# Performance work log

Hardware: AMD Instinct MI355X
Metric: run time of the kernel (lower is better)

Reference implementation:

```python
import jax, jax.numpy as jnp
import numpy as np

N_NODES = 10000


def _sage_conv(x, src, dst, W_l, W_r, b):
    # mean aggregation of source features at destination nodes (PyG SAGEConv default)
    msg = x[src]                                             # [E, C_in]
    agg = jax.ops.segment_sum(msg, dst, num_segments=N_NODES)  # [N, C_in]
    cnt = jax.ops.segment_sum(jnp.ones((src.shape[0],), x.dtype), dst,
                              num_segments=N_NODES)
    mean = agg / jnp.maximum(cnt, 1.0)[:, None]              # isolated nodes -> 0
    return mean @ W_l + x @ W_r + b


def setup_inputs() -> dict:
    key = jax.random.key(0)
    ks = jax.random.split(key, 8)
    E = 640000
    x = jax.random.normal(ks[0], (N_NODES, 128), dtype=jnp.float32)
    edge_index = jax.random.randint(ks[1], (2, E), 0, N_NODES, dtype=jnp.int64)
    W1_l = jax.random.normal(ks[2], (128, 256), dtype=jnp.float32) * 0.05
    W1_r = jax.random.normal(ks[3], (128, 256), dtype=jnp.float32) * 0.05
    b1 = jnp.zeros((256,), dtype=jnp.float32)
    W2_l = jax.random.normal(ks[4], (256, 128), dtype=jnp.float32) * 0.05
    W2_r = jax.random.normal(ks[5], (256, 128), dtype=jnp.float32) * 0.05
    b2 = jnp.zeros((128,), dtype=jnp.float32)
    return {"x": x, "edge_index": edge_index, "W1_l": W1_l, "W1_r": W1_r,
            "b1": b1, "W2_l": W2_l, "W2_r": W2_r, "b2": b2}


def reference(x, edge_index, W1_l, W1_r, b1, W2_l, W2_r, b2):
    src, dst = edge_index[0], edge_index[1]
    h = jax.nn.relu(_sage_conv(x, src, dst, W1_l, W1_r, b1))
    out = _sage_conv(h, src, dst, W2_l, W2_r, b2)
    return out
```

## Files before the change

kernel.cpp:

```cpp
#include <hip/hip_runtime.h>

#define N_NODES 10000
#define HB 128

typedef unsigned int uint;
typedef unsigned short ushort;
typedef __attribute__((ext_vector_type(8))) short bf16x8;
typedef __attribute__((ext_vector_type(4))) float f32x4;

__device__ __forceinline__ ushort f2bf(float f) {
    uint b = __float_as_uint(f);
    b += 0x7fffu + ((b >> 16) & 1u);
    return (ushort)(b >> 16);
}

#define CAST_B 1250
#define TCAST_B 512

__global__ __launch_bounds__(256) void prep_kernel(const float* __restrict__ x,
                                                   const float* __restrict__ W1l,
                                                   const float* __restrict__ W1r,
                                                   const float* __restrict__ W2l,
                                                   const float* __restrict__ W2r,
                                                   const int* __restrict__ dst, int E, int chunk,
                                                   int* __restrict__ chunk_hist,
                                                   ushort* __restrict__ lrank,
                                                   ushort* __restrict__ xb,
                                                   ushort* __restrict__ W1T,
                                                   ushort* __restrict__ W2T,
                                                   int* __restrict__ aggv) {
    __shared__ int hist[N_NODES];
    int b = blockIdx.x;
    int t = threadIdx.x;
    if (b < HB) {
        int4* h4 = (int4*)hist;
        for (int i = t; i < N_NODES / 4; i += 256) h4[i] = make_int4(0, 0, 0, 0);
        __syncthreads();
        int e0 = b * chunk;
        int e1 = e0 + chunk; if (e1 > E) e1 = E;
        for (int e = e0 + t; e < e1; e += 256) {
            int d = dst[e];
            lrank[e] = (ushort)atomicAdd(&hist[d], 1);
        }
        __syncthreads();
        int4* c4 = (int4*)(chunk_hist + b * N_NODES);
        for (int i = t; i < N_NODES / 4; i += 256) c4[i] = h4[i];
    } else if (b < HB + CAST_B) {
        if (b == HB && t < 64) aggv[t] = 0;
        int i = (b - HB) * 256 + t;
        float4 v = ((const float4*)x)[i];
        ushort4 o;
        o.x = f2bf(v.x); o.y = f2bf(v.y); o.z = f2bf(v.z); o.w = f2bf(v.w);
        ((ushort4*)xb)[i] = o;
    } else {
        int id = b - HB - CAST_B;
        int z = id >> 8;
        int c = id & 255;
        int k = t;
        if (z == 0) {
            float v = (k < 128) ? W1l[k * 256 + c] : W1r[(k - 128) * 256 + c];
            W1T[c * 256 + k] = f2bf(v);
        } else {
            float v = (c < 128) ? W2l[k * 128 + c] : W2r[k * 128 + (c - 128)];
            W2T[c * 256 + k] = f2bf(v);
        }
    }
}

__global__ __launch_bounds__(256) void csr_mid_kernel(int* __restrict__ ch,
                                                      int* __restrict__ row_ptr,
                                                      int* __restrict__ aggv) {
    int b = blockIdx.x, t = threadIdx.x;
    int n = b * 256 + t;
    bool ok = n < N_NODES;
    int s = 0;
    if (ok) {
#pragma unroll 8
        for (int c = 0; c < HB; ++c) s += ch[c * N_NODES + n];
    }
    int lane = t & 63, wid = t >> 6;
    int incl = s;
#pragma unroll
    for (int off = 1; off < 64; off <<= 1) {
        int y = __shfl_up(incl, off);
        if (lane >= off) incl += y;
    }
    __shared__ int wsum[4];
    __shared__ int sbase;
    if (lane == 63) wsum[wid] = incl;
    __syncthreads();
    int tot = wsum[0] + wsum[1] + wsum[2] + wsum[3];
    int wbase = 0;
#pragma unroll
    for (int w = 0; w < 4; ++w)
        if (w < wid) wbase += wsum[w];
    incl += wbase;
    if (t == 0)
        __hip_atomic_store(&aggv[b], tot + 1, __ATOMIC_RELEASE, __HIP_MEMORY_SCOPE_AGENT);
    if (t < 64) {
        int v = 0;
        if (t < b) {
            do {
                v = __hip_atomic_load(&aggv[t], __ATOMIC_ACQUIRE, __HIP_MEMORY_SCOPE_AGENT);
            } while (v == 0);
            --v;
        }
#pragma unroll
        for (int m = 1; m < 64; m <<= 1) v += __shfl_xor(v, m);
        if (t == 0) sbase = v;
    }
    __syncthreads();
    int base = sbase;
    if (b == 0 && t == 0) row_ptr[0] = 0;
    if (ok) {
        row_ptr[n + 1] = base + incl;
        int run = base + incl - s;
#pragma unroll 8
        for (int c = 0; c < HB; ++c) {
            int v = ch[c * N_NODES + n];
            ch[c * N_NODES + n] = run;
            run += v;
        }
    }
}

__global__ __launch_bounds__(256) void scatter_kernel(const int* __restrict__ src,
                                                      const int* __restrict__ dst,
                                                      const ushort* __restrict__ lrank,
                                                      const int* __restrict__ off,
                                                      int E, int chunk,
                                                      ushort* __restrict__ csr) {
    int g = blockIdx.x * blockDim.x + threadIdx.x;
    int e = g * 4;
    if (e + 3 < E) {
        int b = e / chunk;
        const int* ob = off + b * N_NODES;
        int4 d = *(const int4*)&dst[e];
        int4 s = *(const int4*)&src[e];
        ushort4 r = *(const ushort4*)&lrank[e];
        csr[ob[d.x] + r.x] = (ushort)s.x;
        csr[ob[d.y] + r.y] = (ushort)s.y;
        csr[ob[d.z] + r.z] = (ushort)s.z;
        csr[ob[d.w] + r.w] = (ushort)s.w;
    } else {
        for (; e < E; ++e)
            csr[off[(e / chunk) * N_NODES + dst[e]] + lrank[e]] = (ushort)src[e];
    }
}

template <int MODE>
__global__ __launch_bounds__(256) void agg_kernel(const ushort* __restrict__ feat,
                                                  const int* __restrict__ row_ptr,
                                                  const ushort* __restrict__ csr,
                                                  uint* __restrict__ outb,
                                                  float* __restrict__ out) {
    int wave = threadIdx.x >> 6;
    int lane = threadIdx.x & 63;
    int n = blockIdx.x * 4 + wave;
    if (n >= N_NODES) return;
    int beg = row_ptr[n], end = row_ptr[n + 1];
    const uint* f = (const uint*)feat;
    float ax0 = 0, ay0 = 0, ax1 = 0, ay1 = 0, ax2 = 0, ay2 = 0, ax3 = 0, ay3 = 0;
    int i = beg;
    for (; i + 8 <= end; i += 8) {
        int s0 = csr[i + 0];
        int s1 = csr[i + 1];
        int s2 = csr[i + 2];
        int s3 = csr[i + 3];
        int s4 = csr[i + 4];
        int s5 = csr[i + 5];
        int s6 = csr[i + 6];
        int s7 = csr[i + 7];
        uint u0 = f[s0 * 64 + lane];
        uint u1 = f[s1 * 64 + lane];
        uint u2 = f[s2 * 64 + lane];
        uint u3 = f[s3 * 64 + lane];
        uint u4 = f[s4 * 64 + lane];
        uint u5 = f[s5 * 64 + lane];
        uint u6 = f[s6 * 64 + lane];
        uint u7 = f[s7 * 64 + lane];
        ax0 += __uint_as_float(u0 << 16); ay0 += __uint_as_float(u0 & 0xffff0000u);
        ax1 += __uint_as_float(u1 << 16); ay1 += __uint_as_float(u1 & 0xffff0000u);
        ax2 += __uint_as_float(u2 << 16); ay2 += __uint_as_float(u2 & 0xffff0000u);
        ax3 += __uint_as_float(u3 << 16); ay3 += __uint_as_float(u3 & 0xffff0000u);
        ax0 += __uint_as_float(u4 << 16); ay0 += __uint_as_float(u4 & 0xffff0000u);
        ax1 += __uint_as_float(u5 << 16); ay1 += __uint_as_float(u5 & 0xffff0000u);
        ax2 += __uint_as_float(u6 << 16); ay2 += __uint_as_float(u6 & 0xffff0000u);
        ax3 += __uint_as_float(u7 << 16); ay3 += __uint_as_float(u7 & 0xffff0000u);
    }
    for (; i + 4 <= end; i += 4) {
        int s0 = csr[i + 0];
        int s1 = csr[i + 1];
        int s2 = csr[i + 2];
        int s3 = csr[i + 3];
        uint u0 = f[s0 * 64 + lane];
        uint u1 = f[s1 * 64 + lane];
        uint u2 = f[s2 * 64 + lane];
        uint u3 = f[s3 * 64 + lane];
        ax0 += __uint_as_float(u0 << 16); ay0 += __uint_as_float(u0 & 0xffff0000u);
        ax1 += __uint_as_float(u1 << 16); ay1 += __uint_as_float(u1 & 0xffff0000u);
        ax2 += __uint_as_float(u2 << 16); ay2 += __uint_as_float(u2 & 0xffff0000u);
        ax3 += __uint_as_float(u3 << 16); ay3 += __uint_as_float(u3 & 0xffff0000u);
    }
    for (; i < end; ++i) {
        int s = csr[i];
        uint u = f[s * 64 + lane];
        ax0 += __uint_as_float(u << 16); ay0 += __uint_as_float(u & 0xffff0000u);
    }
    float deg = (float)(end - beg);
    float inv = deg > 0.f ? 1.0f / deg : 0.0f;
    float sx = ((ax0 + ax1) + (ax2 + ax3)) * inv;
    float sy = ((ay0 + ay1) + (ay2 + ay3)) * inv;
    if (MODE == 0) {
        outb[n * 64 + lane] = (uint)f2bf(sx) | ((uint)f2bf(sy) << 16);
    } else {
        float2* o = (float2*)&out[n * 128 + lane * 2];
        float2 prev = *o;
        prev.x += sx; prev.y += sy;
        *o = prev;
    }
}

__global__ __launch_bounds__(256) void gemm_fused(const ushort* __restrict__ m1b,
                                                  const ushort* __restrict__ xb,
                                                  const ushort* __restrict__ W1T,
                                                  const float* __restrict__ b1,
                                                  const ushort* __restrict__ W2T,
                                                  const float* __restrict__ b2,
                                                  ushort* __restrict__ t,
                                                  float* __restrict__ out) {
    __shared__ ushort hsh[16 * 264];
    int w = threadIdx.x >> 6, lane = threadIdx.x & 63;
    int lr = lane & 15, lg = lane >> 4;
    int r0 = blockIdx.x * 16;
    int row = r0 + lr;
    int c0 = w * 64;

    bf16x8 afr[8];
#pragma unroll
    for (int ks = 0; ks < 8; ++ks) {
        int k0 = ks * 32;
        const ushort* Ab = (k0 < 128) ? (m1b + row * 128 + k0) : (xb + row * 128 + (k0 - 128));
        afr[ks] = *(const bf16x8*)(Ab + lg * 8);
    }

    {
        f32x4 acc[4] = {};
#pragma unroll
        for (int ks = 0; ks < 8; ++ks) {
            int k0 = ks * 32;
#pragma unroll
            for (int cg = 0; cg < 4; ++cg) {
                int col = c0 + cg * 16 + lr;
                bf16x8 b = *(const bf16x8*)(W1T + col * 256 + k0 + lg * 8);
                acc[cg] = __builtin_amdgcn_mfma_f32_16x16x32_bf16(afr[ks], b, acc[cg], 0, 0, 0);
            }
        }
#pragma unroll
        for (int cg = 0; cg < 4; ++cg) {
            int col = c0 + cg * 16 + lr;
            float bias = b1[col];
#pragma unroll
            for (int i = 0; i < 4; ++i) {
                float v = acc[cg][i] + bias;
                v = v > 0.f ? v : 0.f;
                hsh[(lg * 4 + i) * 264 + col] = f2bf(v);
            }
        }
    }
    __syncthreads();

    bf16x8 afr2[8];
#pragma unroll
    for (int ks = 0; ks < 8; ++ks)
        afr2[ks] = *(const bf16x8*)&hsh[lr * 264 + ks * 32 + lg * 8];

    {
        f32x4 acc[4] = {};
#pragma unroll
        for (int ks = 0; ks < 8; ++ks) {
            int k0 = ks * 32;
#pragma unroll
            for (int cg = 0; cg < 4; ++cg) {
                int col = c0 + cg * 16 + lr;
                bf16x8 b = *(const bf16x8*)(W2T + col * 256 + k0 + lg * 8);
                acc[cg] = __builtin_amdgcn_mfma_f32_16x16x32_bf16(afr2[ks], b, acc[cg], 0, 0, 0);
            }
        }
#pragma unroll
        for (int cg = 0; cg < 4; ++cg) {
            int col = c0 + cg * 16 + lr;
            if (col < 128) {
#pragma unroll
                for (int i = 0; i < 4; ++i)
                    t[(r0 + lg * 4 + i) * 128 + col] = f2bf(acc[cg][i]);
            } else {
                int oc = col - 128;
                float bias = b2[oc];
#pragma unroll
                for (int i = 0; i < 4; ++i)
                    out[(r0 + lg * 4 + i) * 128 + oc] = acc[cg][i] + bias;
            }
        }
    }
}


extern "C" void kernel_launch(void* const* d_in, const int* in_sizes, int n_in,
                              void* d_out, int out_size, void* d_ws, size_t ws_size,
                              hipStream_t stream) {
    const float* x   = (const float*)d_in[0];
    const int* edge  = (const int*)d_in[1];
    const float* W1l = (const float*)d_in[2];
    const float* W1r = (const float*)d_in[3];
    const float* b1  = (const float*)d_in[4];
    const float* W2l = (const float*)d_in[5];
    const float* W2r = (const float*)d_in[6];
    const float* b2  = (const float*)d_in[7];
    float* out = (float*)d_out;

    int E = in_sizes[1] / 2;
    const int* src = edge;
    const int* dst = edge + E;
    int chunk = (((E + HB - 1) / HB) + 3) & ~3;

    ushort* m1b  = (ushort*)d_ws;
    ushort* hb   = m1b + (size_t)N_NODES * 128;
    ushort* xb   = hb + (size_t)N_NODES * 256;
    ushort* W1T  = xb + (size_t)N_NODES * 128;
    ushort* W2T  = W1T + 256 * 256;
    ushort* csr  = W2T + 256 * 256;
    ushort* lrank= csr + E;
    int* chist   = (int*)(lrank + E);
    int* row_ptr = chist + HB * N_NODES;
    int* aggv    = row_ptr + (N_NODES + 1);
    ushort* tb   = m1b;

    prep_kernel<<<HB + CAST_B + TCAST_B, 256, 0, stream>>>(x, W1l, W1r, W2l, W2r,
                                                           dst, E, chunk, chist, lrank,
                                                           xb, W1T, W2T, aggv);

    csr_mid_kernel<<<(N_NODES + 255) / 256, 256, 0, stream>>>(chist, row_ptr, aggv);

    scatter_kernel<<<(E / 4 + 255) / 256, 256, 0, stream>>>(src, dst, lrank, chist, E, chunk, csr);

    agg_kernel<0><<<(N_NODES + 3) / 4, 256, 0, stream>>>(xb, row_ptr, csr, (uint*)m1b, nullptr);

    gemm_fused<<<N_NODES / 16, 256, 0, stream>>>(m1b, xb, W1T, b1, W2T, b2, tb, out);

    agg_kernel<1><<<(N_NODES + 3) / 4, 256, 0, stream>>>(tb, row_ptr, csr, nullptr, out);
}
```

Baseline: 100.3 us.

## Fuse first-layer mean aggregation into the fused GEMM kernel

The first-layer neighbor mean aggregation is moved into the GEMM kernel. Each block gathers and averages the neighbors for its 16 rows and stages the result in shared memory as bf16 before the MFMA loop. This removes one kernel launch and the global write and re-read of the intermediate mean buffer. In exchange, the GEMM blocks now run irregular gather work before their matrix multiplies, and there are only 625 such blocks, which may limit latency hiding for the gathers.

Measured after the change: 101.7 us. Within noise of the previous version (+1.4%).

```diff
diff --git a/kernel.cpp b/kernel.cpp
--- a/kernel.cpp
+++ b/kernel.cpp
@@ -14,152 +14,10 @@
     return (ushort)(b >> 16);
 }
 
-#define CAST_B 1250
-#define TCAST_B 512
-
-__global__ __launch_bounds__(256) void prep_kernel(const float* __restrict__ x,
-                                                   const float* __restrict__ W1l,
-                                                   const float* __restrict__ W1r,
-                                                   const float* __restrict__ W2l,
-                                                   const float* __restrict__ W2r,
-                                                   const int* __restrict__ dst, int E, int chunk,
-                                                   int* __restrict__ chunk_hist,
-                                                   ushort* __restrict__ lrank,
-                                                   ushort* __restrict__ xb,
-                                                   ushort* __restrict__ W1T,
-                                                   ushort* __restrict__ W2T,
-                                                   int* __restrict__ aggv) {
-    __shared__ int hist[N_NODES];
-    int b = blockIdx.x;
-    int t = threadIdx.x;
-    if (b < HB) {
-        int4* h4 = (int4*)hist;
-        for (int i = t; i < N_NODES / 4; i += 256) h4[i] = make_int4(0, 0, 0, 0);
-        __syncthreads();
-        int e0 = b * chunk;
-        int e1 = e0 + chunk; if (e1 > E) e1 = E;
-        for (int e = e0 + t; e < e1; e += 256) {
-            int d = dst[e];
-            lrank[e] = (ushort)atomicAdd(&hist[d], 1);
-        }
-        __syncthreads();
-        int4* c4 = (int4*)(chunk_hist + b * N_NODES);
-        for (int i = t; i < N_NODES / 4; i += 256) c4[i] = h4[i];
-    } else if (b < HB + CAST_B) {
-        if (b == HB && t < 64) aggv[t] = 0;
-        int i = (b - HB) * 256 + t;
-        float4 v = ((const float4*)x)[i];
-        ushort4 o;
-        o.x = f2bf(v.x); o.y = f2bf(v.y); o.z = f2bf(v.z); o.w = f2bf(v.w);
-        ((ushort4*)xb)[i] = o;
-    } else {
-        int id = b - HB - CAST_B;
-        int z = id >> 8;
-        int c = id & 255;
-        int k = t;
-        if (z == 0) {
-            float v = (k < 128) ? W1l[k * 256 + c] : W1r[(k - 128) * 256 + c];
-            W1T[c * 256 + k] = f2bf(v);
-        } else {
-            float v = (c < 128) ? W2l[k * 128 + c] : W2r[k * 128 + (c - 128)];
-            W2T[c * 256 + k] = f2bf(v);
-        }
-    }
-}
-
-__global__ __launch_bounds__(256) void csr_mid_kernel(int* __restrict__ ch,
-                                                      int* __restrict__ row_ptr,
-                                                      int* __restrict__ aggv) {
-    int b = blockIdx.x, t = threadIdx.x;
-    int n = b * 256 + t;
-    bool ok = n < N_NODES;
-    int s = 0;
-    if (ok) {
-#pragma unroll 8
-        for (int c = 0; c < HB; ++c) s += ch[c * N_NODES + n];
-    }
-    int lane = t & 63, wid = t >> 6;
-    int incl = s;
-#pragma unroll
-    for (int off = 1; off < 64; off <<= 1) {
-        int y = __shfl_up(incl, off);
-        if (lane >= off) incl += y;
-    }
-    __shared__ int wsum[4];
-    __shared__ int sbase;
-    if (lane == 63) wsum[wid] = incl;
-    __syncthreads();
-    int tot = wsum[0] + wsum[1] + wsum[2] + wsum[3];
-    int wbase = 0;
-#pragma unroll
-    for (int w = 0; w < 4; ++w)
-        if (w < wid) wbase += wsum[w];
-    incl += wbase;
-    if (t == 0)
-        __hip_atomic_store(&aggv[b], tot + 1, __ATOMIC_RELEASE, __HIP_MEMORY_SCOPE_AGENT);
-    if (t < 64) {
-        int v = 0;
-        if (t < b) {
-            do {
-                v = __hip_atomic_load(&aggv[t], __ATOMIC_ACQUIRE, __HIP_MEMORY_SCOPE_AGENT);
-            } while (v == 0);
-            --v;
-        }
-#pragma unroll
-        for (int m = 1; m < 64; m <<= 1) v += __shfl_xor(v, m);
-        if (t == 0) sbase = v;
-    }
-    __syncthreads();
-    int base = sbase;
-    if (b == 0 && t == 0) row_ptr[0] = 0;
-    if (ok) {
-        row_ptr[n + 1] = base + incl;
-        int run = base + incl - s;
-#pragma unroll 8
-        for (int c = 0; c < HB; ++c) {
-            int v = ch[c * N_NODES + n];
-            ch[c * N_NODES + n] = run;
-            run += v;
-        }
-    }
-}
-
-__global__ __launch_bounds__(256) void scatter_kernel(const int* __restrict__ src,
-                                                      const int* __restrict__ dst,
-                                                      const ushort* __restrict__ lrank,
-                                                      const int* __restrict__ off,
-                                                      int E, int chunk,
-                                                      ushort* __restrict__ csr) {
-    int g = blockIdx.x * blockDim.x + threadIdx.x;
-    int e = g * 4;
-    if (e + 3 < E) {
-        int b = e / chunk;
-        const int* ob = off + b * N_NODES;
-        int4 d = *(const int4*)&dst[e];
-        int4 s = *(const int4*)&src[e];
-        ushort4 r = *(const ushort4*)&lrank[e];
-        csr[ob[d.x] + r.x] = (ushort)s.x;
-        csr[ob[d.y] + r.y] = (ushort)s.y;
-        csr[ob[d.z] + r.z] = (ushort)s.z;
-        csr[ob[d.w] + r.w] = (ushort)s.w;
-    } else {
-        for (; e < E; ++e)
-            csr[off[(e / chunk) * N_NODES + dst[e]] + lrank[e]] = (ushort)src[e];
-    }
-}
-
-template <int MODE>
-__global__ __launch_bounds__(256) void agg_kernel(const ushort* __restrict__ feat,
-                                                  const int* __restrict__ row_ptr,
-                                                  const ushort* __restrict__ csr,
-                                                  uint* __restrict__ outb,
-                                                  float* __restrict__ out) {
-    int wave = threadIdx.x >> 6;
-    int lane = threadIdx.x & 63;
-    int n = blockIdx.x * 4 + wave;
-    if (n >= N_NODES) return;
+__device__ __forceinline__ float2 mean_node(int n, int lane, const uint* __restrict__ f,
+                                            const int* __restrict__ row_ptr,
+                                            const ushort* __restrict__ csr) {
     int beg = row_ptr[n], end = row_ptr[n + 1];
-    const uint* f = (const uint*)feat;
     float ax0 = 0, ay0 = 0, ax1 = 0, ay1 = 0, ax2 = 0, ay2 = 0, ax3 = 0, ay3 = 0;
     int i = beg;
     for (; i + 8 <= end; i += 8) {
@@ -209,20 +67,164 @@
     }
     float deg = (float)(end - beg);
     float inv = deg > 0.f ? 1.0f / deg : 0.0f;
-    float sx = ((ax0 + ax1) + (ax2 + ax3)) * inv;
-    float sy = ((ay0 + ay1) + (ay2 + ay3)) * inv;
-    if (MODE == 0) {
-        outb[n * 64 + lane] = (uint)f2bf(sx) | ((uint)f2bf(sy) << 16);
+    float2 r;
+    r.x = ((ax0 + ax1) + (ax2 + ax3)) * inv;
+    r.y = ((ay0 + ay1) + (ay2 + ay3)) * inv;
+    return r;
+}
+
+#define CAST_B 1250
+#define TCAST_B 512
+
+__global__ __launch_bounds__(256) void prep_kernel(const float* __restrict__ x,
+                                                   const float* __restrict__ W1l,
+                                                   const float* __restrict__ W1r,
+                                                   const float* __restrict__ W2l,
+                                                   const float* __restrict__ W2r,
+                                                   const int* __restrict__ dst, int E, int chunk,
+                                                   int* __restrict__ chunk_hist,
+                                                   ushort* __restrict__ lrank,
+                                                   ushort* __restrict__ xb,
+                                                   ushort* __restrict__ W1T,
+                                                   ushort* __restrict__ W2T,
+                                                   int* __restrict__ aggv) {
+    __shared__ int hist[N_NODES];
+    int b = blockIdx.x;
+    int t = threadIdx.x;
+    if (b < HB) {
+        int4* h4 = (int4*)hist;
+        for (int i = t; i < N_NODES / 4; i += 256) h4[i] = make_int4(0, 0, 0, 0);
+        __syncthreads();
+        int e0 = b * chunk;
+        int e1 = e0 + chunk; if (e1 > E) e1 = E;
+        for (int e = e0 + t; e < e1; e += 256) {
+            int d = dst[e];
+            lrank[e] = (ushort)atomicAdd(&hist[d], 1);
+        }
+        __syncthreads();
+        int4* c4 = (int4*)(chunk_hist + b * N_NODES);
+        for (int i = t; i < N_NODES / 4; i += 256) c4[i] = h4[i];
+    } else if (b < HB + CAST_B) {
+        if (b == HB && t < 64) aggv[t] = 0;
+        int i = (b - HB) * 256 + t;
+        float4 v = ((const float4*)x)[i];
+        ushort4 o;
+        o.x = f2bf(v.x); o.y = f2bf(v.y); o.z = f2bf(v.z); o.w = f2bf(v.w);
+        ((ushort4*)xb)[i] = o;
     } else {
-        float2* o = (float2*)&out[n * 128 + lane * 2];
-        float2 prev = *o;
-        prev.x += sx; prev.y += sy;
-        *o = prev;
-    }
-}
-
-__global__ __launch_bounds__(256) void gemm_fused(const ushort* __restrict__ m1b,
-                                                  const ushort* __restrict__ xb,
+        int id = b - HB - CAST_B;
+        int z = id >> 8;
+        int c = id & 255;
+        int k = t;
+        if (z == 0) {
+            float v = (k < 128) ? W1l[k * 256 + c] : W1r[(k - 128) * 256 + c];
+            W1T[c * 256 + k] = f2bf(v);
+        } else {
+            float v = (c < 128) ? W2l[k * 128 + c] : W2r[k * 128 + (c - 128)];
+            W2T[c * 256 + k] = f2bf(v);
+        }
+    }
+}
+
+__global__ __launch_bounds__(256) void csr_mid_kernel(int* __restrict__ ch,
+                                                      int* __restrict__ row_ptr,
+                                                      int* __restrict__ aggv) {
+    int b = blockIdx.x, t = threadIdx.x;
+    int n = b * 256 + t;
+    bool ok = n < N_NODES;
+    int s = 0;
+    if (ok) {
+#pragma unroll 8
+        for (int c = 0; c < HB; ++c) s += ch[c * N_NODES + n];
+    }
+    int lane = t & 63, wid = t >> 6;
+    int incl = s;
+#pragma unroll
+    for (int off = 1; off < 64; off <<= 1) {
+        int y = __shfl_up(incl, off);
+        if (lane >= off) incl += y;
+    }
+    __shared__ int wsum[4];
+    __shared__ int sbase;
+    if (lane == 63) wsum[wid] = incl;
+    __syncthreads();
+    int tot = wsum[0] + wsum[1] + wsum[2] + wsum[3];
+    int wbase = 0;
+#pragma unroll
+    for (int w = 0; w < 4; ++w)
+        if (w < wid) wbase += wsum[w];
+    incl += wbase;
+    if (t == 0)
+        __hip_atomic_store(&aggv[b], tot + 1, __ATOMIC_RELEASE, __HIP_MEMORY_SCOPE_AGENT);
+    if (t < 64) {
+        int v = 0;
+        if (t < b) {
+            do {
+                v = __hip_atomic_load(&aggv[t], __ATOMIC_ACQUIRE, __HIP_MEMORY_SCOPE_AGENT);
+            } while (v == 0);
+            --v;
+        }
+#pragma unroll
+        for (int m = 1; m < 64; m <<= 1) v += __shfl_xor(v, m);
+        if (t == 0) sbase = v;
+    }
+    __syncthreads();
+    int base = sbase;
+    if (b == 0 && t == 0) row_ptr[0] = 0;
+    if (ok) {
+        row_ptr[n + 1] = base + incl;
+        int run = base + incl - s;
+#pragma unroll 8
+        for (int c = 0; c < HB; ++c) {
+            int v = ch[c * N_NODES + n];
+            ch[c * N_NODES + n] = run;
+            run += v;
+        }
+    }
+}
+
+__global__ __launch_bounds__(256) void scatter_kernel(const int* __restrict__ src,
+                                                      const int* __restrict__ dst,
+                                                      const ushort* __restrict__ lrank,
+                                                      const int* __restrict__ off,
+                                                      int E, int chunk,
+                                                      ushort* __restrict__ csr) {
+    int g = blockIdx.x * blockDim.x + threadIdx.x;
+    int e = g * 4;
+    if (e + 3 < E) {
+        int b = e / chunk;
+        const int* ob = off + b * N_NODES;
+        int4 d = *(const int4*)&dst[e];
+        int4 s = *(const int4*)&src[e];
+        ushort4 r = *(const ushort4*)&lrank[e];
+        csr[ob[d.x] + r.x] = (ushort)s.x;
+        csr[ob[d.y] + r.y] = (ushort)s.y;
+        csr[ob[d.z] + r.z] = (ushort)s.z;
+        csr[ob[d.w] + r.w] = (ushort)s.w;
+    } else {
+        for (; e < E; ++e)
+            csr[off[(e / chunk) * N_NODES + dst[e]] + lrank[e]] = (ushort)src[e];
+    }
+}
+
+__global__ __launch_bounds__(256) void agg_kernel(const ushort* __restrict__ feat,
+                                                  const int* __restrict__ row_ptr,
+                                                  const ushort* __restrict__ csr,
+                                                  float* __restrict__ out) {
+    int wave = threadIdx.x >> 6;
+    int lane = threadIdx.x & 63;
+    int n = blockIdx.x * 4 + wave;
+    if (n >= N_NODES) return;
+    float2 m = mean_node(n, lane, (const uint*)feat, row_ptr, csr);
+    float2* o = (float2*)&out[n * 128 + lane * 2];
+    float2 prev = *o;
+    prev.x += m.x; prev.y += m.y;
+    *o = prev;
+}
+
+__global__ __launch_bounds__(256) void gemm_fused(const ushort* __restrict__ xb,
+                                                  const int* __restrict__ row_ptr,
+                                                  const ushort* __restrict__ csr,
                                                   const ushort* __restrict__ W1T,
                                                   const float* __restrict__ b1,
                                                   const ushort* __restrict__ W2T,
@@ -230,18 +232,29 @@
                                                   ushort* __restrict__ t,
                                                   float* __restrict__ out) {
     __shared__ ushort hsh[16 * 264];
+    __shared__ ushort m1sh[16 * 136];
     int w = threadIdx.x >> 6, lane = threadIdx.x & 63;
     int lr = lane & 15, lg = lane >> 4;
     int r0 = blockIdx.x * 16;
     int row = r0 + lr;
     int c0 = w * 64;
 
+#pragma unroll
+    for (int j = 0; j < 4; ++j) {
+        int lrow = w * 4 + j;
+        float2 m = mean_node(r0 + lrow, lane, (const uint*)xb, row_ptr, csr);
+        ((uint*)m1sh)[lrow * 68 + lane] = (uint)f2bf(m.x) | ((uint)f2bf(m.y) << 16);
+    }
+    __syncthreads();
+
     bf16x8 afr[8];
 #pragma unroll
     for (int ks = 0; ks < 8; ++ks) {
         int k0 = ks * 32;
-        const ushort* Ab = (k0 < 128) ? (m1b + row * 128 + k0) : (xb + row * 128 + (k0 - 128));
-        afr[ks] = *(const bf16x8*)(Ab + lg * 8);
+        if (k0 < 128)
+            afr[ks] = *(const bf16x8*)&m1sh[lr * 136 + k0 + lg * 8];
+        else
+            afr[ks] = *(const bf16x8*)(xb + row * 128 + (k0 - 128) + lg * 8);
     }
 
     {
@@ -324,8 +337,8 @@
     const int* dst = edge + E;
     int chunk = (((E + HB - 1) / HB) + 3) & ~3;
 
-    ushort* m1b  = (ushort*)d_ws;
-    ushort* hb   = m1b + (size_t)N_NODES * 128;
+    ushort* tb   = (ushort*)d_ws;
+    ushort* hb   = tb + (size_t)N_NODES * 128;
     ushort* xb   = hb + (size_t)N_NODES * 256;
     ushort* W1T  = xb + (size_t)N_NODES * 128;
     ushort* W2T  = W1T + 256 * 256;
@@ -334,7 +347,6 @@
     int* chist   = (int*)(lrank + E);
     int* row_ptr = chist + HB * N_NODES;
     int* aggv    = row_ptr + (N_NODES + 1);
-    ushort* tb   = m1b;
 
     prep_kernel<<<HB + CAST_B + TCAST_B, 256, 0, stream>>>(x, W1l, W1r, W2l, W2r,
                                                            dst, E, chunk, chist, lrank,
@@ -344,9 +356,7 @@
 
     scatter_kernel<<<(E / 4 + 255) / 256, 256, 0, stream>>>(src, dst, lrank, chist, E, chunk, csr);
 
-    agg_kernel<0><<<(N_NODES + 3) / 4, 256, 0, stream>>>(xb, row_ptr, csr, (uint*)m1b, nullptr);
-
-    gemm_fused<<<N_NODES / 16, 256, 0, stream>>>(m1b, xb, W1T, b1, W2T, b2, tb, out);
-
-    agg_kernel<1><<<(N_NODES + 3) / 4, 256, 0, stream>>>(tb, row_ptr, csr, nullptr, out);
-}
+    gemm_fused<<<N_NODES / 16, 256, 0, stream>>>(xb, row_ptr, csr, W1T, b1, W2T, b2, tb, out);
+
+    agg_kernel<<<(N_NODES + 3) / 4, 256, 0, stream>>>(tb, row_ptr, csr, out);
+}
```
